# Optimization experiments

Measured on AMD Instinct MI355X. Metric: run time of the kernel, lower is better.

The kernel has to match this reference:

```python
import jax, jax.numpy as jnp
import numpy as np
from jax import lax

V, D, H, HD, L, E, HID, TOPK, B, T = 32000, 1024, 16, 64, 2, 4, 2048, 2, 1, 1024
EPS = 1e-8


def setup_inputs() -> dict:
    key = jax.random.key(0)
    ks = jax.random.split(key, 10)
    s = 0.02
    so = 0.02 / np.sqrt(2 * L)  # o_proj / down_proj init std
    return dict(
        idx=jax.random.randint(ks[0], (B, T), 0, V),
        tok_emb=jax.random.normal(ks[1], (V, D), jnp.float32) * s,
        attn_norm_w=jnp.ones((L, D), jnp.float32),
        q_w=jax.random.normal(ks[2], (L, D, D), jnp.float32) * s,
        q_b=jnp.zeros((L, D), jnp.float32),
        kv_w=jax.random.normal(ks[3], (L, D, 2 * D), jnp.float32) * s,
        kv_b=jnp.zeros((L, 2 * D), jnp.float32),
        o_w=jax.random.normal(ks[4], (L, D, D), jnp.float32) * so,
        o_b=jnp.zeros((L, D), jnp.float32),
        ffn_norm_w=jnp.ones((L, D), jnp.float32),
        router_w=jax.random.normal(ks[5], (L, D, E), jnp.float32) * s,
        gate_w=jax.random.normal(ks[6], (L, E, D, HID), jnp.float32) * s,
        up_w=jax.random.normal(ks[7], (L, E, D, HID), jnp.float32) * s,
        down_w=jax.random.normal(ks[8], (L, E, HID, D), jnp.float32) * so,
        lnf_w=jnp.ones((D,), jnp.float32),
    )


def _rms(x, w):
    return x / jnp.sqrt(jnp.mean(x * x, axis=-1, keepdims=True) + EPS) * w


def reference(idx, tok_emb, attn_norm_w, q_w, q_b, kv_w, kv_b, o_w, o_b,
              ffn_norm_w, router_w, gate_w, up_w, down_w, lnf_w):
    x = tok_emb[idx]  # [B,T,D]

    # ALiBi bias and causal mask (built once; block_size == T here)
    slopes = jnp.arange(1, H + 1, dtype=jnp.float32) / H          # [H]
    pos = jnp.arange(T, dtype=jnp.float32)
    alibi = slopes[:, None, None] * (pos[None, None, :] - pos[None, :, None])  # [H,T,T]
    causal = jnp.arange(T)[None, :] > jnp.arange(T)[:, None]      # True above diagonal

    for l in range(L):
        # --- causal self-attention with ALiBi ---
        h = _rms(x, attn_norm_w[l])
        q = (h @ q_w[l] + q_b[l]).reshape(B, T, H, HD)
        kv = (h @ kv_w[l] + kv_b[l]).reshape(B, T, 2, H, HD)
        k, v = kv[:, :, 0], kv[:, :, 1]
        att = jnp.einsum('bqhd,bkhd->bhqk', q, k) * (1.0 / np.sqrt(HD))
        att = att + alibi[None]
        att = jnp.where(causal, -jnp.inf, att)
        a = jax.nn.softmax(att, axis=-1)
        y = jnp.einsum('bhqk,bkhd->bqhd', a, v).reshape(B, T, D)
        x = x + y @ o_w[l] + o_b[l]

        # --- MoE FFN (top-k routing, SwiGLU experts, depth-scaled down_proj) ---
        hm = _rms(x, ffn_norm_w[l]).reshape(B * T, D)             # [N,D]
        rlog = hm @ router_w[l]                                   # [N,E]
        vals, sel = lax.top_k(rlog, TOPK)                         # [N,K]
        w = jax.nn.softmax(vals.astype(jnp.float32), axis=-1).astype(hm.dtype)
        # dense per-expert compute, combined sparsely via routing weights
        g = jax.nn.silu(jnp.einsum('nd,edh->enh', hm, gate_w[l])) \
            * jnp.einsum('nd,edh->enh', hm, up_w[l])              # [E,N,HID]
        out_e = jnp.einsum('enh,ehd->end', g, down_w[l]) * (1.0 / np.sqrt(l + 1))
        combine = jnp.sum(jax.nn.one_hot(sel, E, dtype=hm.dtype) * w[..., None], axis=1)  # [N,E]
        moe = jnp.einsum('ne,end->nd', combine, out_e).reshape(B, T, D)
        x = x + moe

    logits = _rms(x, lnf_w) @ tok_emb.T  # tied head weight
    return logits
```

## Files before the change

kernel.cpp:

```cpp
#include <hip/hip_runtime.h>
#include <cmath>

typedef __attribute__((ext_vector_type(8))) _Float16 f16x8;
typedef __attribute__((ext_vector_type(8))) unsigned short u16x8;
typedef __attribute__((ext_vector_type(4))) float f32x4;

#define DEV static __device__ __forceinline__

constexpr int Dm   = 1024;
constexpr int HIDm = 2048;
constexpr int NT   = 1024;
constexpr int NV   = 32000;
constexpr float EPSf  = 1e-8f;
constexpr float LOSC  = 4096.0f;
constexpr float ILOSC = 1.0f / 4096.0f;

DEV unsigned short h2u(_Float16 h){ union{_Float16 h; unsigned short u;} v; v.h=h; return v.u; }

DEV f32x4 MF(f16x8 a, f16x8 b, f32x4 c){ return __builtin_amdgcn_mfma_f32_16x16x32_f16(a,b,c,0,0,0); }

typedef __attribute__((address_space(1))) void GV;
typedef __attribute__((address_space(3))) void LV;
DEV void gll16(const void* g, void* l){
  __builtin_amdgcn_global_load_lds((GV*)(__UINTPTR_TYPE__)g, (LV*)l, 16, 0, 0);
}

DEV int swk(int lane){ return (((lane&3) ^ ((lane>>3)&3))*8); }
DEV int rdc(int fr, int fg){ return ((fg ^ ((fr>>1)&3))*8); }

template<int SPLIT>
DEV void st_sp(unsigned short* __restrict__ hi, unsigned short* __restrict__ lo, size_t o, float v){
  _Float16 hh = (_Float16)v;
  hi[o] = h2u(hh);
  if constexpr (SPLIT==3) lo[o] = h2u((_Float16)((v - (float)hh)*LOSC));
}

__global__ __launch_bounds__(256) void k_init(
    const int* __restrict__ idx, const float* __restrict__ emb,
    float* __restrict__ x, unsigned short* __restrict__ emb16, int gbase)
{
  const int b = blockIdx.x;
  if (b < gbase){
    const size_t i = ((size_t)b*256 + threadIdx.x)*8;
    const float4 v0 = *(const float4*)&emb[i];
    const float4 v1 = *(const float4*)&emb[i+4];
    u16x8 h;
    h[0]=h2u((_Float16)v0.x); h[1]=h2u((_Float16)v0.y);
    h[2]=h2u((_Float16)v0.z); h[3]=h2u((_Float16)v0.w);
    h[4]=h2u((_Float16)v1.x); h[5]=h2u((_Float16)v1.y);
    h[6]=h2u((_Float16)v1.z); h[7]=h2u((_Float16)v1.w);
    *(u16x8*)&emb16[i] = h;
  } else {
    const int t = b - gbase;
    const int d = threadIdx.x*4;
    *(float4*)&x[(size_t)t*Dm + d] = *(const float4*)&emb[(size_t)idx[t]*Dm + d];
  }
}

template<int SPLIT>
__global__ __launch_bounds__(256) void k_rms(
    const float* __restrict__ x, const float* __restrict__ w,
    unsigned short* __restrict__ ohi, unsigned short* __restrict__ olo)
{
  const int t = blockIdx.x, tid = threadIdx.x;
  const float* row = x + (size_t)t*Dm;
  float s = 0.f;
  #pragma unroll
  for (int i=0;i<4;++i){ const float v = row[tid + i*256]; s += v*v; }
  #pragma unroll
  for (int d=1; d<64; d<<=1) s += __shfl_xor(s, d);
  __shared__ float red[4];
  if ((tid&63)==0) red[tid>>6] = s;
  __syncthreads();
  const float tot = red[0]+red[1]+red[2]+red[3];
  const float rstd = rsqrtf(tot*(1.0f/Dm) + EPSf);
  #pragma unroll
  for (int i=0;i<4;++i){
    const int c = tid + i*256;
    st_sp<SPLIT>(ohi, olo, (size_t)t*Dm + c, row[c]*rstd*w[c]);
  }
}

template<int SPLIT>
__global__ __launch_bounds__(256) void k_fuse_o(
    const float* __restrict__ part, const float* __restrict__ ob,
    const float* __restrict__ fnw, const float* __restrict__ rw,
    float* __restrict__ x, unsigned short* __restrict__ hhi,
    unsigned short* __restrict__ hlo, float* __restrict__ cmb)
{
  const int t = blockIdx.x, tid = threadIdx.x, wv = tid>>6, lane = tid&63;
  const int c = tid*4;
  float4 s = *(float4*)&x[(size_t)t*Dm + c];
  #pragma unroll
  for (int z=0; z<4; ++z){
    const float4 p = *(const float4*)&part[((size_t)z*NT + t)*Dm + c];
    s.x+=p.x; s.y+=p.y; s.z+=p.z; s.w+=p.w;
  }
  const float4 b4 = *(const float4*)&ob[c];
  s.x+=b4.x; s.y+=b4.y; s.z+=b4.z; s.w+=b4.w;
  *(float4*)&x[(size_t)t*Dm + c] = s;

  float ss = s.x*s.x + s.y*s.y + s.z*s.z + s.w*s.w;
  #pragma unroll
  for (int d=1; d<64; d<<=1) ss += __shfl_xor(ss, d);
  __shared__ float red[4];
  if (lane==0) red[wv] = ss;
  __syncthreads();
  const float rstd = rsqrtf((red[0]+red[1]+red[2]+red[3])*(1.0f/Dm) + EPSf);

  const float4 w4 = *(const float4*)&fnw[c];
  const float sv[4] = {s.x,s.y,s.z,s.w};
  const float wv4[4] = {w4.x,w4.y,w4.z,w4.w};
  float hm[4];
  float lg[4] = {0.f,0.f,0.f,0.f};
  #pragma unroll
  for (int j=0;j<4;++j){
    hm[j] = sv[j]*rstd*wv4[j];
    st_sp<SPLIT>(hhi, hlo, (size_t)t*Dm + c + j, hm[j]);
    const float4 r4 = *(const float4*)&rw[(size_t)(c+j)*4];
    lg[0] += hm[j]*r4.x; lg[1] += hm[j]*r4.y; lg[2] += hm[j]*r4.z; lg[3] += hm[j]*r4.w;
  }
  #pragma unroll
  for (int d=1; d<64; d<<=1){
    lg[0]+=__shfl_xor(lg[0],d); lg[1]+=__shfl_xor(lg[1],d);
    lg[2]+=__shfl_xor(lg[2],d); lg[3]+=__shfl_xor(lg[3],d);
  }
  __shared__ float red2[4][4];
  if (lane==0){ red2[wv][0]=lg[0]; red2[wv][1]=lg[1]; red2[wv][2]=lg[2]; red2[wv][3]=lg[3]; }
  __syncthreads();
  if (tid==0){
    float L[4];
    #pragma unroll
    for (int e=0;e<4;++e) L[e] = red2[0][e]+red2[1][e]+red2[2][e]+red2[3][e];
    int s0 = 0;
    for (int e=1;e<4;++e) if (L[e] > L[s0]) s0 = e;
    int s1 = -1;
    for (int e=0;e<4;++e){ if (e==s0) continue; if (s1<0 || L[e] > L[s1]) s1 = e; }
    const float eb2 = expf(L[s1] - L[s0]);
    const float inv = 1.0f/(1.0f + eb2);
    float o[4] = {0.f,0.f,0.f,0.f};
    o[s0] = inv; o[s1] = eb2*inv;
    cmb[t*4+0]=o[0]; cmb[t*4+1]=o[1]; cmb[t*4+2]=o[2]; cmb[t*4+3]=o[3];
  }
}

__global__ __launch_bounds__(256) void k_fuse_moe(
    const float* __restrict__ part, const float* __restrict__ cmb,
    const float* __restrict__ w, float* __restrict__ x,
    unsigned short* __restrict__ dst, int writex)
{
  const int t = blockIdx.x, tid = threadIdx.x, wv = tid>>6, lane = tid&63;
  const int c = tid*4;
  float4 s = *(float4*)&x[(size_t)t*Dm + c];
  #pragma unroll
  for (int e=0; e<4; ++e){
    if (cmb[(size_t)t*4 + e] > 0.f){
      const float4 p0 = *(const float4*)&part[((size_t)(e*2+0)*NT + t)*Dm + c];
      const float4 p1 = *(const float4*)&part[((size_t)(e*2+1)*NT + t)*Dm + c];
      s.x+=p0.x+p1.x; s.y+=p0.y+p1.y; s.z+=p0.z+p1.z; s.w+=p0.w+p1.w;
    }
  }
  if (writex) *(float4*)&x[(size_t)t*Dm + c] = s;
  float ss = s.x*s.x + s.y*s.y + s.z*s.z + s.w*s.w;
  #pragma unroll
  for (int d=1; d<64; d<<=1) ss += __shfl_xor(ss, d);
  __shared__ float red[4];
  if (lane==0) red[wv] = ss;
  __syncthreads();
  const float rstd = rsqrtf((red[0]+red[1]+red[2]+red[3])*(1.0f/Dm) + EPSf);
  const float4 w4 = *(const float4*)&w[c];
  const float sv[4] = {s.x,s.y,s.z,s.w};
  const float wv4[4] = {w4.x,w4.y,w4.z,w4.w};
  #pragma unroll
  for (int j=0;j<4;++j)
    dst[(size_t)t*Dm + c + j] = h2u((_Float16)(sv[j]*rstd*wv4[j]));
}

__global__ __launch_bounds__(256) void k_scan(
    const float* __restrict__ cmb, int* __restrict__ tl,
    float* __restrict__ cwl, int* __restrict__ cnt)
{
  const int e = threadIdx.x>>6, lane = threadIdx.x&63;
  int base = 0;
  for (int t0=0; t0<NT; t0+=64){
    const float w = cmb[(size_t)(t0+lane)*4 + e];
    const unsigned long long m = __ballot(w > 0.f);
    const int pre = __popcll(m & ((1ull<<lane)-1ull));
    if (w > 0.f){ tl[e*NT + base + pre] = t0+lane; cwl[e*NT + base + pre] = w; }
    base += __popcll(m);
  }
  if (lane==0) cnt[e] = base;
}

template<int SPLIT>
DEV void wconv_tile(const float* __restrict__ W, unsigned short* __restrict__ Whi,
                    unsigned short* __restrict__ Wlo, int K, int N, int n0, int k0,
                    float (*tile)[65], int t)
{
  const int r = t>>2;
  #pragma unroll
  for (int i=0;i<4;++i){
    const int c = (t&3)*16 + i*4;
    *(float4*)&tile[r][c] = *(const float4*)&W[(size_t)(k0+r)*N + n0 + c];
  }
  __syncthreads();
  const int n = t>>2;
  #pragma unroll
  for (int i=0;i<2;++i){
    const int kc = (t&3)*8 + i*32;
    u16x8 hi, lo;
    #pragma unroll
    for (int j=0;j<8;++j){
      const float v = tile[kc+j][n];
      const _Float16 hh = (_Float16)v;
      hi[j] = h2u(hh);
      if constexpr (SPLIT==3) lo[j] = h2u((_Float16)((v-(float)hh)*LOSC));
      else lo[j] = 0;
    }
    *(u16x8*)&Whi[(size_t)(n0+n)*K + k0 + kc] = hi;
    if constexpr (SPLIT==3) *(u16x8*)&Wlo[(size_t)(n0+n)*K + k0 + kc] = lo;
  }
}

template<int SPLIT>
__global__ __launch_bounds__(256) void k_wconv(
    const float* __restrict__ W, unsigned short* __restrict__ Whi,
    unsigned short* __restrict__ Wlo, int K, int N)
{
  __shared__ float tile[64][65];
  const size_t eb = (size_t)blockIdx.z * (size_t)K * N;
  wconv_tile<SPLIT>(W + eb, Whi + eb, Wlo + eb, K, N, blockIdx.x*64, blockIdx.y*64,
                    tile, threadIdx.x);
}

template<int SPLIT>
__global__ __launch_bounds__(256) void k_wconv_qkvo(
    const float* __restrict__ qw, const float* __restrict__ kvw, const float* __restrict__ ow,
    unsigned short* __restrict__ Wh, unsigned short* __restrict__ Wl,
    unsigned short* __restrict__ WOh, unsigned short* __restrict__ WOl)
{
  __shared__ float tile[64][65];
  const int b = blockIdx.x, t = threadIdx.x;
  if (b < 256){
    wconv_tile<SPLIT>(qw, Wh, Wl, Dm, Dm, (b&15)*64, (b>>4)*64, tile, t);
  } else if (b < 768){
    const int c = b - 256;
    wconv_tile<SPLIT>(kvw, Wh + (size_t)Dm*Dm, Wl + (size_t)Dm*Dm,
                      Dm, 2*Dm, (c&31)*64, (c>>5)*64, tile, t);
  } else {
    const int c = b - 768;
    wconv_tile<SPLIT>(ow, WOh, WOl, Dm, Dm, (c&15)*64, (c>>4)*64, tile, t);
  }
}

template<int SPLIT>
__global__ __launch_bounds__(256) void k_wconv_gu(
    const float* __restrict__ gw, const float* __restrict__ uw,
    unsigned short* __restrict__ WGh, unsigned short* __restrict__ WGl,
    unsigned short* __restrict__ WUh, unsigned short* __restrict__ WUl)
{
  __shared__ float tile[64][65];
  const int b = blockIdx.x, t = threadIdx.x;
  const int half = b >> 11;
  const int c = b & 2047;
  const int e = c >> 9, cc = c & 511;
  const size_t eb = (size_t)e * (size_t)Dm * HIDm;
  const int n0 = (cc&31)*64, k0 = (cc>>5)*64;
  if (half == 0)
    wconv_tile<SPLIT>(gw + eb, WGh + eb, WGl + eb, Dm, HIDm, n0, k0, tile, t);
  else
    wconv_tile<SPLIT>(uw + eb, WUh + eb, WUl + eb, Dm, HIDm, n0, k0, tile, t);
}

template<int SPLIT, int ZMODE>
__global__ __launch_bounds__(256) void k_mm(
    const unsigned short* __restrict__ Ahi, const unsigned short* __restrict__ Alo,
    const unsigned short* __restrict__ Bhi, const unsigned short* __restrict__ Blo,
    float* __restrict__ part, int lda, int ldb, int K, int ldo)
{
  constexpr int PL = (SPLIT==3)?2:1;
  __shared__ __align__(16) unsigned short As[PL][128][32];
  __shared__ __align__(16) unsigned short Bs[PL][128][32];
  const int tid=threadIdx.x, wv=tid>>6, lane=tid&63, fr=lane&15, fg=lane>>4;
  const int n0=blockIdx.x*128, r0=blockIdx.y*128, zz=blockIdx.z;
  const int wr=(wv>>1)*64, wc=(wv&1)*64;
  const int sr=lane>>2, sk=swk(lane);
  const int rc = rdc(fr, fg);

  const f32x4 z4={0.f,0.f,0.f,0.f};
  f32x4 accM[4][4], accC[4][4];
  #pragma unroll
  for (int i=0;i<4;++i)
    #pragma unroll
    for (int j=0;j<4;++j){ accM[i][j]=z4; accC[i][j]=z4; }

  for (int kt=0; kt<K; kt+=32){
    #pragma unroll
    for (int i=0;i<2;++i){
      const int rr = wv*32 + i*16 + sr;
      size_t ao, bo;
      if constexpr (ZMODE==2){
        ao = (size_t)(r0+rr)*lda + zz*K + kt + sk;
        bo = (size_t)(n0+rr)*ldb + zz*K + kt + sk;
      } else {
        ao = (size_t)(r0+rr)*lda + kt + sk;
        bo = (size_t)(n0+rr)*ldb + kt + sk;
      }
      gll16(&Ahi[ao], &As[0][wv*32+i*16][0]);
      if constexpr (SPLIT==3) gll16(&Alo[ao], &As[1][wv*32+i*16][0]);
      gll16(&Bhi[bo], &Bs[0][wv*32+i*16][0]);
      if constexpr (SPLIT==3) gll16(&Blo[bo], &Bs[1][wv*32+i*16][0]);
    }
    __syncthreads();
    f16x8 a[4][PL], b[4][PL];
    #pragma unroll
    for (int rt=0;rt<4;++rt)
      #pragma unroll
      for (int p=0;p<PL;++p) a[rt][p] = *(const f16x8*)&As[p][wr+rt*16+fr][rc];
    #pragma unroll
    for (int ct=0;ct<4;++ct)
      #pragma unroll
      for (int p=0;p<PL;++p) b[ct][p] = *(const f16x8*)&Bs[p][wc+ct*16+fr][rc];
    #pragma unroll
    for (int rt=0;rt<4;++rt)
      #pragma unroll
      for (int ct=0;ct<4;++ct){
        accM[rt][ct] = MF(a[rt][0], b[ct][0], accM[rt][ct]);
        if constexpr (SPLIT==3){
          accC[rt][ct] = MF(a[rt][0], b[ct][1], accC[rt][ct]);
          accC[rt][ct] = MF(a[rt][1], b[ct][0], accC[rt][ct]);
        }
      }
    __syncthreads();
  }

  #pragma unroll
  for (int rt=0;rt<4;++rt)
    #pragma unroll
    for (int ct=0;ct<4;++ct)
      #pragma unroll
      for (int j=0;j<4;++j){
        const int row = r0 + wr + rt*16 + fg*4 + j;
        const int col = n0 + wc + ct*16 + fr;
        float v = accM[rt][ct][j];
        if constexpr (SPLIT==3) v += accC[rt][ct][j]*ILOSC;
        part[((size_t)zz*NT + row)*ldo + col] = v;
      }
}

template<int SPLIT>
__global__ __launch_bounds__(256) void k_comb_qkvt(
    const float* __restrict__ part, const float* __restrict__ qb, const float* __restrict__ kvb,
    unsigned short* __restrict__ qhi, unsigned short* __restrict__ qlo,
    unsigned short* __restrict__ khi, unsigned short* __restrict__ klo,
    unsigned short* __restrict__ vthi, unsigned short* __restrict__ vtlo)
{
  __shared__ float tile[64][65];
  const int bid = blockIdx.x, tid = threadIdx.x;
  if (bid < 1024){
    const int t = bid;
    #pragma unroll
    for (int i=0;i<2;++i){
      const int col = tid*4 + i*1024;
      const float4 p0 = *(const float4*)&part[(size_t)t*3072 + col];
      const float4 p1 = *(const float4*)&part[((size_t)NT + t)*3072 + col];
      float v[4] = {p0.x+p1.x, p0.y+p1.y, p0.z+p1.z, p0.w+p1.w};
      #pragma unroll
      for (int j=0;j<4;++j){
        const int c = col + j;
        if (c < Dm) st_sp<SPLIT>(qhi, qlo, (size_t)t*Dm + c, v[j] + qb[c]);
        else        st_sp<SPLIT>(khi, klo, (size_t)t*Dm + (c-Dm), v[j] + kvb[c-Dm]);
      }
    }
  } else {
    const int c = bid - 1024;
    const int d0 = (c&15)*64, t0 = (c>>4)*64;
    {
      const int tl_ = tid>>2, dc = (tid&3)*16;
      #pragma unroll
      for (int i=0;i<4;++i){
        const int d = dc + i*4;
        const float4 p0 = *(const float4*)&part[(size_t)(t0+tl_)*3072 + 2048 + d0 + d];
        const float4 p1 = *(const float4*)&part[((size_t)NT + t0+tl_)*3072 + 2048 + d0 + d];
        tile[tl_][d+0] = p0.x+p1.x + kvb[1024+d0+d+0];
        tile[tl_][d+1] = p0.y+p1.y + kvb[1024+d0+d+1];
        tile[tl_][d+2] = p0.z+p1.z + kvb[1024+d0+d+2];
        tile[tl_][d+3] = p0.w+p1.w + kvb[1024+d0+d+3];
      }
    }
    __syncthreads();
    #pragma unroll
    for (int i=0;i<2;++i){
      const int u = tid + i*256;
      const int dl = u>>3, tch = (u&7)*8;
      u16x8 hi, lo;
      #pragma unroll
      for (int j=0;j<8;++j){
        const float v = tile[tch+j][dl];
        const _Float16 hh = (_Float16)v;
        hi[j] = h2u(hh);
        if constexpr (SPLIT==3) lo[j] = h2u((_Float16)((v-(float)hh)*LOSC));
        else lo[j] = 0;
      }
      *(u16x8*)&vthi[(size_t)(d0+dl)*NT + t0 + tch] = hi;
      if constexpr (SPLIT==3) *(u16x8*)&vtlo[(size_t)(d0+dl)*NT + t0 + tch] = lo;
    }
  }
}

template<int SPLIT>
__global__ __launch_bounds__(256) void k_down(
    const unsigned short* __restrict__ Ahi, const unsigned short* __restrict__ Alo,
    const unsigned short* __restrict__ Bhi, const unsigned short* __restrict__ Blo,
    const int* __restrict__ tl, const int* __restrict__ cnt,
    float* __restrict__ part)
{
  constexpr int PL = (SPLIT==3)?2:1;
  const int zz = blockIdx.z, e = zz>>1, ks = zz&1;
  const int r0 = blockIdx.y*128, n0 = blockIdx.x*128;
  const int cn = cnt[e];
  if (r0 >= cn) return;
  __shared__ __align__(16) unsigned short As[PL][128][32];
  __shared__ __align__(16) unsigned short Bs[PL][128][32];
  __shared__ int tl_s[128];
  const int tid=threadIdx.x, wv=tid>>6, lane=tid&63, fr=lane&15, fg=lane>>4;
  const int wr=(wv>>1)*64, wc=(wv&1)*64;
  const int sr=lane>>2, sk=swk(lane);
  const int rc = rdc(fr, fg);
  if (tid < 128) tl_s[tid] = (r0+tid < cn) ? tl[e*NT + r0 + tid] : -1;

  const f32x4 z4={0.f,0.f,0.f,0.f};
  f32x4 accM[4][4], accC[4][4];
  #pragma unroll
  for (int i=0;i<4;++i)
    #pragma unroll
    for (int j=0;j<4;++j){ accM[i][j]=z4; accC[i][j]=z4; }

  const int kbeg = ks*1024, kend = kbeg + 1024;
  for (int kt=kbeg; kt<kend; kt+=32){
    #pragma unroll
    for (int i=0;i<2;++i){
      const int rr = wv*32 + i*16 + sr;
      const size_t ao = (size_t)((e<<10) + r0 + rr)*HIDm + kt + sk;
      const size_t bo = (size_t)e*((size_t)Dm*HIDm) + (size_t)(n0+rr)*HIDm + kt + sk;
      gll16(&Ahi[ao], &As[0][wv*32+i*16][0]);
      if constexpr (SPLIT==3) gll16(&Alo[ao], &As[1][wv*32+i*16][0]);
      gll16(&Bhi[bo], &Bs[0][wv*32+i*16][0]);
      if constexpr (SPLIT==3) gll16(&Blo[bo], &Bs[1][wv*32+i*16][0]);
    }
    __syncthreads();
    f16x8 a[4][PL], b[4][PL];
    #pragma unroll
    for (int rt=0;rt<4;++rt)
      #pragma unroll
      for (int p=0;p<PL;++p) a[rt][p] = *(const f16x8*)&As[p][wr+rt*16+fr][rc];
    #pragma unroll
    for (int ct=0;ct<4;++ct)
      #pragma unroll
      for (int p=0;p<PL;++p) b[ct][p] = *(const f16x8*)&Bs[p][wc+ct*16+fr][rc];
    #pragma unroll
    for (int rt=0;rt<4;++rt)
      #pragma unroll
      for (int ct=0;ct<4;++ct){
        accM[rt][ct] = MF(a[rt][0], b[ct][0], accM[rt][ct]);
        if constexpr (SPLIT==3){
          accC[rt][ct] = MF(a[rt][0], b[ct][1], accC[rt][ct]);
          accC[rt][ct] = MF(a[rt][1], b[ct][0], accC[rt][ct]);
        }
      }
    __syncthreads();
  }

  #pragma unroll
  for (int rt=0;rt<4;++rt)
    #pragma unroll
    for (int ct=0;ct<4;++ct)
      #pragma unroll
      for (int j=0;j<4;++j){
        const int i = wr + rt*16 + fg*4 + j;
        const int col = n0 + wc + ct*16 + fr;
        float v = accM[rt][ct][j];
        if constexpr (SPLIT==3) v += accC[rt][ct][j]*ILOSC;
        const int tok = tl_s[i];
        if (tok >= 0) part[((size_t)zz*NT + tok)*Dm + col] = v;
      }
}

template<int SPLIT>
__global__ __launch_bounds__(512) void k_guf(
    const unsigned short* __restrict__ Ahi, const unsigned short* __restrict__ Alo,
    const unsigned short* __restrict__ Ghi, const unsigned short* __restrict__ Glo,
    const unsigned short* __restrict__ Uhi, const unsigned short* __restrict__ Ulo,
    const int* __restrict__ tl, const float* __restrict__ cwl, const int* __restrict__ cnt,
    unsigned short* __restrict__ Hhi, unsigned short* __restrict__ Hlo, float scale)
{
  constexpr int PL=(SPLIT==3)?2:1;
  const int e = blockIdx.z, r0 = blockIdx.y*128, n0 = blockIdx.x*64;
  const int cn = cnt[e];
  if (r0 >= cn) return;
  __shared__ __align__(16) unsigned short As[PL][128][32];
  __shared__ __align__(16) unsigned short Gs[PL][64][32];
  __shared__ __align__(16) unsigned short Us[PL][64][32];
  __shared__ float cw_s[128];
  const int tid=threadIdx.x, wv=tid>>6, lane=tid&63, fr=lane&15, fg=lane>>4;
  const int wr=(wv>>1)*32, wc=(wv&1)*32;
  const int sr=lane>>2, sk=swk(lane);
  const int rc = rdc(fr, fg);
  const size_t ebW = (size_t)e * ((size_t)HIDm*Dm);
  if (tid < 128) cw_s[tid] = (r0+tid < cn) ? cwl[e*NT + r0 + tid]*scale : 0.f;

  const int lrA = r0 + wv*16 + sr;
  const int tokA = tl[e*NT + (lrA < cn ? lrA : cn-1)];
  const size_t abase = (size_t)tokA*Dm + sk;
  const int rrB = (wv&3)*16 + sr;
  const size_t bbase = ebW + (size_t)(n0+rrB)*Dm + sk;

  const f32x4 z4={0.f,0.f,0.f,0.f};
  f32x4 aGM[2][2],aGC[2][2],aUM[2][2],aUC[2][2];
  #pragma unroll
  for (int i=0;i<2;++i)
    #pragma unroll
    for (int j=0;j<2;++j){ aGM[i][j]=z4; aGC[i][j]=z4; aUM[i][j]=z4; aUC[i][j]=z4; }

  for (int kt=0; kt<Dm; kt+=32){
    gll16(&Ahi[abase + kt], &As[0][wv*16][0]);
    if constexpr (SPLIT==3) gll16(&Alo[abase + kt], &As[1][wv*16][0]);
    if (wv < 4){
      gll16(&Ghi[bbase + kt], &Gs[0][(wv&3)*16][0]);
      if constexpr (SPLIT==3) gll16(&Glo[bbase + kt], &Gs[1][(wv&3)*16][0]);
    } else {
      gll16(&Uhi[bbase + kt], &Us[0][(wv&3)*16][0]);
      if constexpr (SPLIT==3) gll16(&Ulo[bbase + kt], &Us[1][(wv&3)*16][0]);
    }
    __syncthreads();
    f16x8 a[2][PL], bg[2][PL], bu[2][PL];
    #pragma unroll
    for (int rt=0;rt<2;++rt)
      #pragma unroll
      for (int p=0;p<PL;++p) a[rt][p] = *(const f16x8*)&As[p][wr+rt*16+fr][rc];
    #pragma unroll
    for (int ct=0;ct<2;++ct)
      #pragma unroll
      for (int p=0;p<PL;++p){
        bg[ct][p] = *(const f16x8*)&Gs[p][wc+ct*16+fr][rc];
        bu[ct][p] = *(const f16x8*)&Us[p][wc+ct*16+fr][rc];
      }
    #pragma unroll
    for (int rt=0;rt<2;++rt)
      #pragma unroll
      for (int ct=0;ct<2;++ct){
        aGM[rt][ct] = MF(a[rt][0], bg[ct][0], aGM[rt][ct]);
        aUM[rt][ct] = MF(a[rt][0], bu[ct][0], aUM[rt][ct]);
        if constexpr (SPLIT==3){
          aGC[rt][ct] = MF(a[rt][0], bg[ct][1], aGC[rt][ct]);
          aGC[rt][ct] = MF(a[rt][1], bg[ct][0], aGC[rt][ct]);
          aUC[rt][ct] = MF(a[rt][0], bu[ct][1], aUC[rt][ct]);
          aUC[rt][ct] = MF(a[rt][1], bu[ct][0], aUC[rt][ct]);
        }
      }
    __syncthreads();
  }
  #pragma unroll
  for (int rt=0;rt<2;++rt)
    #pragma unroll
    for (int ct=0;ct<2;++ct)
      #pragma unroll
      for (int j=0;j<4;++j){
        const int i = wr + rt*16 + fg*4 + j;
        const int row = r0 + i;
        const int col = n0 + wc + ct*16 + fr;
        float g = aGM[rt][ct][j], u = aUM[rt][ct][j];
        if constexpr (SPLIT==3){ g += aGC[rt][ct][j]*ILOSC; u += aUC[rt][ct][j]*ILOSC; }
        const float cw = cw_s[i];
        const float h = (g/(1.0f + expf(-g))) * u * cw;
        st_sp<SPLIT>(Hhi, Hlo, (size_t)((e<<10) + row)*HIDm + col, h);
      }
}

__global__ __launch_bounds__(256) void k_lg(
    const unsigned short* __restrict__ Ahi, const float* __restrict__ emb,
    float* __restrict__ out)
{
  __shared__ __align__(16) unsigned short As[128][32];
  __shared__ __align__(16) unsigned short Bs[128][32];
  const int tid=threadIdx.x, wv=tid>>6, lane=tid&63, fr=lane&15, fg=lane>>4;
  const int w = (blockIdx.x & 7)*250 + (blockIdx.x >> 3);
  const int n0 = (w>>3)*128, r0 = (w&7)*128;
  const int wr=(wv>>1)*64, wc=(wv&1)*64;
  const int sr=lane>>2, sk=swk(lane);
  const int rc = rdc(fr, fg);
  const int br = tid>>1;
  const f32x4 z4={0.f,0.f,0.f,0.f};
  f32x4 acc[4][4];
  #pragma unroll
  for (int i=0;i<4;++i)
    #pragma unroll
    for (int j=0;j<4;++j) acc[i][j]=z4;

  for (int kt=0; kt<Dm; kt+=32){
    #pragma unroll
    for (int i=0;i<2;++i){
      const int rr = wv*32 + i*16 + sr;
      gll16(&Ahi[(size_t)(r0+rr)*Dm + kt + sk], &As[wv*32+i*16][0]);
    }
    {
      const int bc = (tid&1)*16;
      const float* s = &emb[(size_t)(n0+br)*Dm + kt + bc];
      const float4 v0 = *(const float4*)s;
      const float4 v1 = *(const float4*)(s+4);
      const float4 v2 = *(const float4*)(s+8);
      const float4 v3 = *(const float4*)(s+12);
      u16x8 h0, h1;
      h0[0]=h2u((_Float16)v0.x); h0[1]=h2u((_Float16)v0.y);
      h0[2]=h2u((_Float16)v0.z); h0[3]=h2u((_Float16)v0.w);
      h0[4]=h2u((_Float16)v1.x); h0[5]=h2u((_Float16)v1.y);
      h0[6]=h2u((_Float16)v1.z); h0[7]=h2u((_Float16)v1.w);
      h1[0]=h2u((_Float16)v2.x); h1[1]=h2u((_Float16)v2.y);
      h1[2]=h2u((_Float16)v2.z); h1[3]=h2u((_Float16)v2.w);
      h1[4]=h2u((_Float16)v3.x); h1[5]=h2u((_Float16)v3.y);
      h1[6]=h2u((_Float16)v3.z); h1[7]=h2u((_Float16)v3.w);
      const int s_ = (br>>1)&3;
      const int u0 = (tid&1)*2;
      *(u16x8*)&Bs[br][(u0^s_)*8]     = h0;
      *(u16x8*)&Bs[br][((u0+1)^s_)*8] = h1;
    }
    __syncthreads();
    f16x8 a[4], b[4];
    #pragma unroll
    for (int rt=0;rt<4;++rt) a[rt] = *(const f16x8*)&As[wr+rt*16+fr][rc];
    #pragma unroll
    for (int ct=0;ct<4;++ct) b[ct] = *(const f16x8*)&Bs[wc+ct*16+fr][rc];
    #pragma unroll
    for (int rt=0;rt<4;++rt)
      #pragma unroll
      for (int ct=0;ct<4;++ct) acc[rt][ct] = MF(a[rt], b[ct], acc[rt][ct]);
    __syncthreads();
  }
  #pragma unroll
  for (int rt=0;rt<4;++rt)
    #pragma unroll
    for (int ct=0;ct<4;++ct)
      #pragma unroll
      for (int j=0;j<4;++j)
        out[(size_t)(r0+wr+rt*16+fg*4+j)*NV + n0+wc+ct*16+fr] = acc[rt][ct][j];
}

__global__ __launch_bounds__(256) void k_lg16(
    const unsigned short* __restrict__ Ahi, const unsigned short* __restrict__ B16,
    float* __restrict__ out)
{
  __shared__ __align__(16) unsigned short As[128][64];
  __shared__ __align__(16) unsigned short Bs[128][64];
  const int tid=threadIdx.x, wv=tid>>6, lane=tid&63, fr=lane&15, fg=lane>>4;
  const int w = (blockIdx.x & 7)*250 + (blockIdx.x >> 3);
  const int n0 = (w>>3)*128, r0 = (w&7)*128;
  const int wr=(wv>>1)*64, wc=(wv&1)*64;
  const int srow = lane>>3;
  const int sk = (((lane&7) ^ srow)*8);
  const f32x4 z4={0.f,0.f,0.f,0.f};
  f32x4 acc[4][4];
  #pragma unroll
  for (int i=0;i<4;++i)
    #pragma unroll
    for (int j=0;j<4;++j) acc[i][j]=z4;

  for (int kt=0; kt<Dm; kt+=64){
    #pragma unroll
    for (int i=0;i<4;++i){
      const int rr = wv*32 + i*8 + srow;
      gll16(&Ahi[(size_t)(r0+rr)*Dm + kt + sk], &As[wv*32+i*8][0]);
      gll16(&B16[(size_t)(n0+rr)*Dm + kt + sk], &Bs[wv*32+i*8][0]);
    }
    __syncthreads();
    f16x8 a[4][2], b[4][2];
    #pragma unroll
    for (int rt=0;rt<4;++rt)
      #pragma unroll
      for (int kk=0;kk<2;++kk)
        a[rt][kk] = *(const f16x8*)&As[wr+rt*16+fr][(((kk*4+fg) ^ (fr&7))*8)];
    #pragma unroll
    for (int ct=0;ct<4;++ct)
      #pragma unroll
      for (int kk=0;kk<2;++kk)
        b[ct][kk] = *(const f16x8*)&Bs[wc+ct*16+fr][(((kk*4+fg) ^ (fr&7))*8)];
    #pragma unroll
    for (int rt=0;rt<4;++rt)
      #pragma unroll
      for (int ct=0;ct<4;++ct){
        acc[rt][ct] = MF(a[rt][0], b[ct][0], acc[rt][ct]);
        acc[rt][ct] = MF(a[rt][1], b[ct][1], acc[rt][ct]);
      }
    __syncthreads();
  }
  #pragma unroll
  for (int rt=0;rt<4;++rt)
    #pragma unroll
    for (int ct=0;ct<4;++ct)
      #pragma unroll
      for (int j=0;j<4;++j)
        out[(size_t)(r0+wr+rt*16+fg*4+j)*NV + n0+wc+ct*16+fr] = acc[rt][ct][j];
}

template<int SPLIT>
__global__ __launch_bounds__(256) void k_attn(
    const unsigned short* __restrict__ qhi, const unsigned short* __restrict__ qlo,
    const unsigned short* __restrict__ khi, const unsigned short* __restrict__ klo,
    const unsigned short* __restrict__ vthi, const unsigned short* __restrict__ vtlo,
    unsigned short* __restrict__ yhi, unsigned short* __restrict__ ylo)
{
  constexpr int PL = (SPLIT==3) ? 2 : 1;
  const int qt = blockIdx.x, hd = blockIdx.y;
  const int tid = threadIdx.x, wv = tid>>6, lane = tid&63;
  const int fr = lane&15, fg = lane>>4;
  const int rbase = qt*64 + wv*16;
  const float slope = (float)(hd+1) * (1.0f/16.0f);

  __shared__ __align__(16) unsigned short Ps[4][PL][16][32];

  f16x8 aq[2][PL];
  #pragma unroll
  for (int c=0;c<2;++c){
    const size_t off = (size_t)(rbase+fr)*Dm + hd*64 + c*32 + fg*8;
    aq[c][0] = *(const f16x8*)&qhi[off];
    if constexpr (SPLIT==3) aq[c][1] = *(const f16x8*)&qlo[off];
  }

  const f32x4 z4 = {0.f,0.f,0.f,0.f};
  f32x4 yM[4], yC[4];
  #pragma unroll
  for (int ct=0;ct<4;++ct){ yM[ct]=z4; yC[ct]=z4; }
  float m[4], lsum[4];
  #pragma unroll
  for (int j=0;j<4;++j){ m[j] = -INFINITY; lsum[j] = 0.f; }

  const int nkt = qt*2 + 2;
  for (int kt=0; kt<nkt; ++kt){
    f32x4 sM[2], sC[2];
    sM[0]=z4; sM[1]=z4; sC[0]=z4; sC[1]=z4;
    #pragma unroll
    for (int kh=0; kh<2; ++kh){
      #pragma unroll
      for (int c=0;c<2;++c){
        const size_t off = (size_t)(kt*32 + kh*16 + fr)*Dm + hd*64 + c*32 + fg*8;
        const f16x8 b0 = *(const f16x8*)&khi[off];
        sM[kh] = MF(aq[c][0], b0, sM[kh]);
        if constexpr (SPLIT==3){
          const f16x8 b1 = *(const f16x8*)&klo[off];
          sC[kh] = MF(aq[c][0], b1, sC[kh]);
          sC[kh] = MF(aq[c][1], b0, sC[kh]);
        }
      }
    }
    float sv[2][4], mx[4];
    #pragma unroll
    for (int j=0;j<4;++j) mx[j] = -INFINITY;
    #pragma unroll
    for (int kh=0; kh<2; ++kh)
      #pragma unroll
      for (int j=0;j<4;++j){
        const int kcol = kt*32 + kh*16 + fr;
        const int row  = rbase + fg*4 + j;
        float s = sM[kh][j];
        if constexpr (SPLIT==3) s += sC[kh][j]*ILOSC;
        s = s*0.125f + slope*(float)(kcol - row);
        sv[kh][j] = (kcol > row) ? -INFINITY : s;
        mx[j] = fmaxf(mx[j], sv[kh][j]);
      }
    #pragma unroll
    for (int d=1; d<16; d<<=1)
      #pragma unroll
      for (int j=0;j<4;++j) mx[j] = fmaxf(mx[j], __shfl_xor(mx[j], d));
    float resc[4];
    #pragma unroll
    for (int j=0;j<4;++j){
      const float mn = fmaxf(m[j], mx[j]);
      resc[j] = expf(m[j] - mn);
      m[j] = mn;
    }
    float p[2][4], psum[4];
    #pragma unroll
    for (int j=0;j<4;++j) psum[j] = 0.f;
    #pragma unroll
    for (int kh=0;kh<2;++kh)
      #pragma unroll
      for (int j=0;j<4;++j){
        const float pv = (sv[kh][j] == -INFINITY) ? 0.f : expf(sv[kh][j] - m[j]);
        p[kh][j] = pv; psum[j] += pv;
      }
    #pragma unroll
    for (int d=1; d<16; d<<=1)
      #pragma unroll
      for (int j=0;j<4;++j) psum[j] += __shfl_xor(psum[j], d);
    #pragma unroll
    for (int j=0;j<4;++j) lsum[j] = lsum[j]*resc[j] + psum[j];
    #pragma unroll
    for (int ct=0;ct<4;++ct)
      #pragma unroll
      for (int j=0;j<4;++j){ yM[ct][j]*=resc[j]; yC[ct][j]*=resc[j]; }
    #pragma unroll
    for (int kh=0;kh<2;++kh)
      #pragma unroll
      for (int j=0;j<4;++j){
        const float pv = p[kh][j];
        _Float16 ph = (_Float16)pv;
        Ps[wv][0][fg*4+j][kh*16+fr] = h2u(ph);
        if constexpr (SPLIT==3)
          Ps[wv][1][fg*4+j][kh*16+fr] = h2u((_Float16)((pv-(float)ph)*LOSC));
      }
    asm volatile("s_waitcnt lgkmcnt(0)" ::: "memory");
    f16x8 pa[PL];
    pa[0] = *(const f16x8*)&Ps[wv][0][fr][fg*8];
    if constexpr (SPLIT==3) pa[1] = *(const f16x8*)&Ps[wv][1][fr][fg*8];
    #pragma unroll
    for (int ct=0;ct<4;++ct){
      const size_t off = (size_t)(hd*64 + ct*16 + fr)*NT + kt*32 + fg*8;
      const f16x8 v0 = *(const f16x8*)&vthi[off];
      yM[ct] = MF(pa[0], v0, yM[ct]);
      if constexpr (SPLIT==3){
        const f16x8 v1 = *(const f16x8*)&vtlo[off];
        yC[ct] = MF(pa[0], v1, yC[ct]);
        yC[ct] = MF(pa[1], v0, yC[ct]);
      }
    }
    asm volatile("s_waitcnt lgkmcnt(0)" ::: "memory");
  }
  #pragma unroll
  for (int ct=0;ct<4;++ct)
    #pragma unroll
    for (int j=0;j<4;++j){
      float v = yM[ct][j];
      if constexpr (SPLIT==3) v += yC[ct][j]*ILOSC;
      v /= lsum[j];
      const size_t off = (size_t)(rbase + fg*4 + j)*Dm + hd*64 + ct*16 + fr;
      st_sp<SPLIT>(yhi, ylo, off, v);
    }
}

struct Ptrs {
  float* x; float* cmb; float* part; float* cwl; int* tl; int* cnt;
  unsigned short *hhi,*hlo,*qhi,*qlo,*khi,*klo,*vthi,*vtlo,*yhi,*ylo,*Hhi,*Hlo;
  unsigned short *Wqkvh,*Wqkvl,*WOh,*WOl,*WGh,*WGl,*WUh,*WUl,*WDh,*WDl;
};

template<int S>
static void run_layer(const Ptrs& P, int l,
    const float* anw, const float* qw, const float* qb, const float* kvw, const float* kvb,
    const float* ow, const float* ob, const float* fnw, const float* rw,
    const float* gw, const float* uw, const float* dw,
    const float* nextw, unsigned short* nextdst, int writex, float scale, hipStream_t stream)
{
  (void)anw;
  k_wconv_qkvo<S><<<dim3(1024), dim3(256), 0, stream>>>(
      qw + (size_t)l*Dm*Dm, kvw + (size_t)l*Dm*2*Dm, ow + (size_t)l*Dm*Dm,
      P.Wqkvh, P.Wqkvl, P.WOh, P.WOl);
  k_mm<S,2><<<dim3(24,8,2), dim3(256), 0, stream>>>(P.hhi, P.hlo, P.Wqkvh, P.Wqkvl,
      P.part, Dm, Dm, 512, 3072);
  k_comb_qkvt<S><<<dim3(1280), dim3(256), 0, stream>>>(P.part, qb + l*Dm, kvb + l*2*Dm,
      P.qhi, P.qlo, P.khi, P.klo, P.vthi, P.vtlo);
  k_attn<S><<<dim3(16,16), dim3(256), 0, stream>>>(P.qhi,P.qlo,P.khi,P.klo,P.vthi,P.vtlo,P.yhi,P.ylo);
  k_mm<S,2><<<dim3(8,8,4), dim3(256), 0, stream>>>(P.yhi, P.ylo, P.WOh, P.WOl,
      P.part, Dm, Dm, 256, Dm);
  k_fuse_o<S><<<dim3(NT), dim3(256), 0, stream>>>(P.part, ob + l*Dm, fnw + l*Dm,
      rw + (size_t)l*Dm*4, P.x, P.hhi, P.hlo, P.cmb);
  k_scan<<<dim3(1), dim3(256), 0, stream>>>(P.cmb, P.tl, P.cwl, P.cnt);
  k_wconv_gu<S><<<dim3(4096), dim3(256), 0, stream>>>(
      gw + (size_t)l*4*Dm*HIDm, uw + (size_t)l*4*Dm*HIDm, P.WGh, P.WGl, P.WUh, P.WUl);
  k_guf<S><<<dim3(32,8,4), dim3(512), 0, stream>>>(P.hhi, P.hlo, P.WGh, P.WGl, P.WUh, P.WUl,
      P.tl, P.cwl, P.cnt, P.Hhi, P.Hlo, scale);
  k_wconv<S><<<dim3(16,32,4), dim3(256), 0, stream>>>(dw + (size_t)l*4*HIDm*Dm, P.WDh, P.WDl, HIDm, Dm);
  k_down<S><<<dim3(8,8,8), dim3(256), 0, stream>>>(P.Hhi, P.Hlo, P.WDh, P.WDl,
      P.tl, P.cnt, P.part);
  k_fuse_moe<<<dim3(NT), dim3(256), 0, stream>>>(P.part, P.cmb, nextw, P.x, nextdst, writex);
}

extern "C" void kernel_launch(void* const* d_in, const int* in_sizes, int n_in,
                              void* d_out, int out_size, void* d_ws, size_t ws_size,
                              hipStream_t stream)
{
  (void)in_sizes; (void)n_in; (void)out_size;
  const int*   idx = (const int*)d_in[0];
  const float* emb = (const float*)d_in[1];
  const float* anw = (const float*)d_in[2];
  const float* qw  = (const float*)d_in[3];
  const float* qb  = (const float*)d_in[4];
  const float* kvw = (const float*)d_in[5];
  const float* kvb = (const float*)d_in[6];
  const float* ow  = (const float*)d_in[7];
  const float* ob  = (const float*)d_in[8];
  const float* fnw = (const float*)d_in[9];
  const float* rw  = (const float*)d_in[10];
  const float* gw  = (const float*)d_in[11];
  const float* uw  = (const float*)d_in[12];
  const float* dw  = (const float*)d_in[13];
  const float* lnf = (const float*)d_in[14];

  constexpr size_t MB = (size_t)1<<20;
  constexpr size_t KB = (size_t)1<<10;
  char* sc = (char*)d_out;
  Ptrs P;
  P.x     = (float*)sc;
  P.hhi   = (unsigned short*)(sc + 4*MB);
  P.hlo   = (unsigned short*)(sc + 6*MB);
  P.qhi   = (unsigned short*)(sc + 8*MB);
  P.qlo   = (unsigned short*)(sc + 10*MB);
  P.khi   = (unsigned short*)(sc + 12*MB);
  P.klo   = (unsigned short*)(sc + 14*MB);
  P.vthi  = (unsigned short*)(sc + 16*MB);
  P.vtlo  = (unsigned short*)(sc + 18*MB);
  P.yhi   = (unsigned short*)(sc + 20*MB);
  P.ylo   = (unsigned short*)(sc + 22*MB);
  P.cmb   = (float*)(sc + 24*MB);
  P.tl    = (int*)(sc + 24*MB + 64*KB);
  P.cwl   = (float*)(sc + 24*MB + 128*KB);
  P.cnt   = (int*)(sc + 24*MB + 192*KB);
  P.Hhi   = (unsigned short*)(sc + 25*MB);
  P.Hlo   = (unsigned short*)(sc + 41*MB);
  P.Wqkvh = (unsigned short*)(sc + 57*MB);
  P.Wqkvl = (unsigned short*)(sc + 63*MB);
  P.WOh   = (unsigned short*)(sc + 69*MB);
  P.WOl   = (unsigned short*)(sc + 71*MB);
  P.WGh   = (unsigned short*)(sc + 57*MB);
  P.WGl   = (unsigned short*)(sc + 73*MB);
  P.WUh   = (unsigned short*)(sc + 89*MB);
  P.WUl   = (unsigned short*)(sc + 105*MB);
  P.WDh   = (unsigned short*)(sc + 57*MB);
  P.WDl   = (unsigned short*)(sc + 73*MB);
  P.part  = (float*)(sc + 89*MB);
  unsigned short* xhat  = (unsigned short*)d_ws;
  unsigned short* emb16 = (unsigned short*)((char*)d_ws + 2*MB);
  const bool big_ws = ws_size >= 68*MB;
  float* out = (float*)d_out;

  const int gbase = big_ws ? 16000 : 0;
  k_init<<<dim3(gbase + NT), dim3(256), 0, stream>>>(idx, emb, P.x, emb16, gbase);
  k_rms<3><<<dim3(NT), dim3(256), 0, stream>>>(P.x, anw, P.hhi, P.hlo);

  run_layer<3>(P, 0, anw, qw, qb, kvw, kvb, ow, ob, fnw, rw, gw, uw, dw,
               anw + Dm, P.hhi, 1, 1.0f, stream);
  run_layer<1>(P, 1, anw, qw, qb, kvw, kvb, ow, ob, fnw, rw, gw, uw, dw,
               lnf, xhat, 0, 0.70710678f, stream);

  if (big_ws)
    k_lg16<<<dim3(2000), dim3(256), 0, stream>>>(xhat, emb16, out);
  else
    k_lg<<<dim3(2000), dim3(256), 0, stream>>>(xhat, emb, out);
}
```

Baseline: 794.9 us.

## Remap GEMM grids for XCD-aware L2 locality and enlarge logits tiles

```diff
diff --git a/kernel.cpp b/kernel.cpp
--- a/kernel.cpp
+++ b/kernel.cpp
@@ -276,13 +276,16 @@
 __global__ __launch_bounds__(256) void k_mm(
     const unsigned short* __restrict__ Ahi, const unsigned short* __restrict__ Alo,
     const unsigned short* __restrict__ Bhi, const unsigned short* __restrict__ Blo,
-    float* __restrict__ part, int lda, int ldb, int K, int ldo)
+    float* __restrict__ part, int lda, int ldb, int K, int ldo, int nx)
 {
   constexpr int PL = (SPLIT==3)?2:1;
   __shared__ __align__(16) unsigned short As[PL][128][32];
   __shared__ __align__(16) unsigned short Bs[PL][128][32];
+  const int xcd = blockIdx.x & 7, ii = blockIdx.x >> 3;
+  const int w = xcd * (int)(gridDim.x >> 3) + ii;
+  const int g = w >> 3, yy = w & 7;
+  const int n0 = (g % nx)*128, r0 = yy*128, zz = g / nx;
   const int tid=threadIdx.x, wv=tid>>6, lane=tid&63, fr=lane&15, fg=lane>>4;
-  const int n0=blockIdx.x*128, r0=blockIdx.y*128, zz=blockIdx.z;
   const int wr=(wv>>1)*64, wc=(wv&1)*64;
   const int sr=lane>>2, sk=swk(lane);
   const int rc = rdc(fr, fg);
@@ -416,8 +419,11 @@
     float* __restrict__ part)
 {
   constexpr int PL = (SPLIT==3)?2:1;
-  const int zz = blockIdx.z, e = zz>>1, ks = zz&1;
-  const int r0 = blockIdx.y*128, n0 = blockIdx.x*128;
+  const int xcd = blockIdx.x & 7, ii = blockIdx.x >> 3;
+  const int w = xcd*64 + ii;
+  const int g = w >> 3, yy = w & 7;
+  const int zz = g >> 3, e = zz >> 1, ks = zz & 1;
+  const int r0 = yy*128, n0 = (g&7)*128;
   const int cn = cnt[e];
   if (r0 >= cn) return;
   __shared__ __align__(16) unsigned short As[PL][128][32];
@@ -495,7 +501,10 @@
     unsigned short* __restrict__ Hhi, unsigned short* __restrict__ Hlo, float scale)
 {
   constexpr int PL=(SPLIT==3)?2:1;
-  const int e = blockIdx.z, r0 = blockIdx.y*128, n0 = blockIdx.x*64;
+  const int xcd = blockIdx.x & 7, ii = blockIdx.x >> 3;
+  const int w = xcd*128 + ii;
+  const int g = w >> 3, yy = w & 7;
+  const int e = g >> 5, n0 = (g & 31)*64, r0 = yy*128;
   const int cn = cnt[e];
   if (r0 >= cn) return;
   __shared__ __align__(16) unsigned short As[PL][128][32];
@@ -569,10 +578,10 @@
         const int i = wr + rt*16 + fg*4 + j;
         const int row = r0 + i;
         const int col = n0 + wc + ct*16 + fr;
-        float g = aGM[rt][ct][j], u = aUM[rt][ct][j];
-        if constexpr (SPLIT==3){ g += aGC[rt][ct][j]*ILOSC; u += aUC[rt][ct][j]*ILOSC; }
+        float g2 = aGM[rt][ct][j], u = aUM[rt][ct][j];
+        if constexpr (SPLIT==3){ g2 += aGC[rt][ct][j]*ILOSC; u += aUC[rt][ct][j]*ILOSC; }
         const float cw = cw_s[i];
-        const float h = (g/(1.0f + expf(-g))) * u * cw;
+        const float h = (g2/(1.0f + expf(-g2))) * u * cw;
         st_sp<SPLIT>(Hhi, Hlo, (size_t)((e<<10) + row)*HIDm + col, h);
       }
 }
@@ -645,22 +654,23 @@
         out[(size_t)(r0+wr+rt*16+fg*4+j)*NV + n0+wc+ct*16+fr] = acc[rt][ct][j];
 }
 
-__global__ __launch_bounds__(256) void k_lg16(
+__global__ __launch_bounds__(512) void k_lg16(
     const unsigned short* __restrict__ Ahi, const unsigned short* __restrict__ B16,
     float* __restrict__ out)
 {
-  __shared__ __align__(16) unsigned short As[128][64];
-  __shared__ __align__(16) unsigned short Bs[128][64];
+  __shared__ __align__(16) unsigned short As[256][64];
+  __shared__ __align__(16) unsigned short Bs[256][64];
   const int tid=threadIdx.x, wv=tid>>6, lane=tid&63, fr=lane&15, fg=lane>>4;
-  const int w = (blockIdx.x & 7)*250 + (blockIdx.x >> 3);
-  const int n0 = (w>>3)*128, r0 = (w&7)*128;
-  const int wr=(wv>>1)*64, wc=(wv&1)*64;
+  const int xcd = blockIdx.x & 7, ii = blockIdx.x >> 3;
+  const int w = (xcd < 4 ? xcd*63 : 252 + (xcd-4)*62) + ii;
+  const int n0 = (w>>2)*256, r0 = (w&3)*256;
+  const int wrow=(wv>>2)*128, wcol=(wv&3)*64;
   const int srow = lane>>3;
   const int sk = (((lane&7) ^ srow)*8);
   const f32x4 z4={0.f,0.f,0.f,0.f};
-  f32x4 acc[4][4];
-  #pragma unroll
-  for (int i=0;i<4;++i)
+  f32x4 acc[8][4];
+  #pragma unroll
+  for (int i=0;i<8;++i)
     #pragma unroll
     for (int j=0;j<4;++j) acc[i][j]=z4;
 
@@ -672,33 +682,29 @@
       gll16(&B16[(size_t)(n0+rr)*Dm + kt + sk], &Bs[wv*32+i*8][0]);
     }
     __syncthreads();
-    f16x8 a[4][2], b[4][2];
-    #pragma unroll
-    for (int rt=0;rt<4;++rt)
-      #pragma unroll
-      for (int kk=0;kk<2;++kk)
-        a[rt][kk] = *(const f16x8*)&As[wr+rt*16+fr][(((kk*4+fg) ^ (fr&7))*8)];
+    #pragma unroll
+    for (int kk=0;kk<2;++kk){
+      f16x8 a[8], b[4];
+      #pragma unroll
+      for (int rt=0;rt<8;++rt)
+        a[rt] = *(const f16x8*)&As[wrow+rt*16+fr][(((kk*4+fg) ^ (fr&7))*8)];
+      #pragma unroll
+      for (int ct=0;ct<4;++ct)
+        b[ct] = *(const f16x8*)&Bs[wcol+ct*16+fr][(((kk*4+fg) ^ (fr&7))*8)];
+      #pragma unroll
+      for (int rt=0;rt<8;++rt)
+        #pragma unroll
+        for (int ct=0;ct<4;++ct) acc[rt][ct] = MF(a[rt], b[ct], acc[rt][ct]);
+    }
+    __syncthreads();
+  }
+  #pragma unroll
+  for (int rt=0;rt<8;++rt)
     #pragma unroll
     for (int ct=0;ct<4;++ct)
       #pragma unroll
-      for (int kk=0;kk<2;++kk)
-        b[ct][kk] = *(const f16x8*)&Bs[wc+ct*16+fr][(((kk*4+fg) ^ (fr&7))*8)];
-    #pragma unroll
-    for (int rt=0;rt<4;++rt)
-      #pragma unroll
-      for (int ct=0;ct<4;++ct){
-        acc[rt][ct] = MF(a[rt][0], b[ct][0], acc[rt][ct]);
-        acc[rt][ct] = MF(a[rt][1], b[ct][1], acc[rt][ct]);
-      }
-    __syncthreads();
-  }
-  #pragma unroll
-  for (int rt=0;rt<4;++rt)
-    #pragma unroll
-    for (int ct=0;ct<4;++ct)
-      #pragma unroll
       for (int j=0;j<4;++j)
-        out[(size_t)(r0+wr+rt*16+fg*4+j)*NV + n0+wc+ct*16+fr] = acc[rt][ct][j];
+        out[(size_t)(r0+wrow+rt*16+fg*4+j)*NV + n0+wcol+ct*16+fr] = acc[rt][ct][j];
 }
 
 template<int SPLIT>
@@ -853,22 +859,22 @@
   k_wconv_qkvo<S><<<dim3(1024), dim3(256), 0, stream>>>(
       qw + (size_t)l*Dm*Dm, kvw + (size_t)l*Dm*2*Dm, ow + (size_t)l*Dm*Dm,
       P.Wqkvh, P.Wqkvl, P.WOh, P.WOl);
-  k_mm<S,2><<<dim3(24,8,2), dim3(256), 0, stream>>>(P.hhi, P.hlo, P.Wqkvh, P.Wqkvl,
-      P.part, Dm, Dm, 512, 3072);
+  k_mm<S,2><<<dim3(384), dim3(256), 0, stream>>>(P.hhi, P.hlo, P.Wqkvh, P.Wqkvl,
+      P.part, Dm, Dm, 512, 3072, 24);
   k_comb_qkvt<S><<<dim3(1280), dim3(256), 0, stream>>>(P.part, qb + l*Dm, kvb + l*2*Dm,
       P.qhi, P.qlo, P.khi, P.klo, P.vthi, P.vtlo);
   k_attn<S><<<dim3(16,16), dim3(256), 0, stream>>>(P.qhi,P.qlo,P.khi,P.klo,P.vthi,P.vtlo,P.yhi,P.ylo);
-  k_mm<S,2><<<dim3(8,8,4), dim3(256), 0, stream>>>(P.yhi, P.ylo, P.WOh, P.WOl,
-      P.part, Dm, Dm, 256, Dm);
+  k_mm<S,2><<<dim3(256), dim3(256), 0, stream>>>(P.yhi, P.ylo, P.WOh, P.WOl,
+      P.part, Dm, Dm, 256, Dm, 8);
   k_fuse_o<S><<<dim3(NT), dim3(256), 0, stream>>>(P.part, ob + l*Dm, fnw + l*Dm,
       rw + (size_t)l*Dm*4, P.x, P.hhi, P.hlo, P.cmb);
   k_scan<<<dim3(1), dim3(256), 0, stream>>>(P.cmb, P.tl, P.cwl, P.cnt);
   k_wconv_gu<S><<<dim3(4096), dim3(256), 0, stream>>>(
       gw + (size_t)l*4*Dm*HIDm, uw + (size_t)l*4*Dm*HIDm, P.WGh, P.WGl, P.WUh, P.WUl);
-  k_guf<S><<<dim3(32,8,4), dim3(512), 0, stream>>>(P.hhi, P.hlo, P.WGh, P.WGl, P.WUh, P.WUl,
+  k_guf<S><<<dim3(1024), dim3(512), 0, stream>>>(P.hhi, P.hlo, P.WGh, P.WGl, P.WUh, P.WUl,
       P.tl, P.cwl, P.cnt, P.Hhi, P.Hlo, scale);
   k_wconv<S><<<dim3(16,32,4), dim3(256), 0, stream>>>(dw + (size_t)l*4*HIDm*Dm, P.WDh, P.WDl, HIDm, Dm);
-  k_down<S><<<dim3(8,8,8), dim3(256), 0, stream>>>(P.Hhi, P.Hlo, P.WDh, P.WDl,
+  k_down<S><<<dim3(512), dim3(256), 0, stream>>>(P.Hhi, P.Hlo, P.WDh, P.WDl,
       P.tl, P.cnt, P.part);
   k_fuse_moe<<<dim3(NT), dim3(256), 0, stream>>>(P.part, P.cmb, nextw, P.x, nextdst, writex);
 }
@@ -941,7 +947,7 @@
                lnf, xhat, 0, 0.70710678f, stream);
 
   if (big_ws)
-    k_lg16<<<dim3(2000), dim3(256), 0, stream>>>(xhat, emb16, out);
+    k_lg16<<<dim3(500), dim3(512), 0, stream>>>(xhat, emb16, out);
   else
     k_lg<<<dim3(2000), dim3(256), 0, stream>>>(xhat, emb, out);
 }
```

Result: slower. 812.8 us (+2.3%).
